# Performance work log

Measured on AMD Instinct MI355X. Metric: run time of the kernel, lower is better.

## Reference

```python
import jax, jax.numpy as jnp
import numpy as np

NUM_NETWORKS = 1024
IN_FEATURES = 32
OUT_FEATURES = 32
POINTS_PER_NET = 128
TOTAL_POINTS = NUM_NETWORKS * POINTS_PER_NET  # 131072


def setup_inputs() -> dict:
    key = jax.random.key(0)
    k1, k2, k3 = jax.random.split(key, 3)
    x = jax.random.normal(k1, (TOTAL_POINTS, IN_FEATURES), dtype=jnp.float32)
    # per-network weight matrices [N, in, out] and biases [N, out]
    weights = jax.random.normal(k2, (NUM_NETWORKS, IN_FEATURES, OUT_FEATURES), dtype=jnp.float32) * 0.1
    biases = jax.random.normal(k3, (NUM_NETWORKS, OUT_FEATURES), dtype=jnp.float32) * 0.1
    # contiguous point counts per network (static/uniform here, matching sum == TOTAL_POINTS)
    batch_size_per_network = jnp.full((NUM_NETWORKS,), POINTS_PER_NET, dtype=jnp.int32)
    return {"x": x, "weights": weights, "biases": biases,
            "batch_size_per_network": batch_size_per_network}


def reference(x, weights, biases, batch_size_per_network):
    # Grouped batched matmul: points are laid out contiguously per network.
    # seg[t] = network id owning point t.
    n = weights.shape[0]
    total = x.shape[0]
    seg = jnp.repeat(jnp.arange(n, dtype=jnp.int32), batch_size_per_network,
                     total_repeat_length=total)  # [total]
    # y_t = x_t @ W[seg_t] + b[seg_t]
    w_t = weights[seg]                     # [total, in, out] (gathered per point)
    y = jnp.einsum('ti,tio->to', x, w_t) + biases[seg]
    return y
```

## Files before the change

kernel.cpp:

```cpp
#include <hip/hip_runtime.h>


#define BLK 128

__global__ __launch_bounds__(BLK) void mnl_kernel(
    const float* __restrict__ x,
    const float* __restrict__ w,
    const float* __restrict__ bias,
    const int* __restrict__ cnt,
    float* __restrict__ y)
{
    __shared__ float xT[32][BLK];
    __shared__ float Wl[32][32];
    __shared__ float Bl[32];
    __shared__ int   red[BLK];

    const int n = blockIdx.x;
    const int t = threadIdx.x;

    int s = 0;
    for (int j = t; j < n; j += BLK) s += cnt[j];
    red[t] = s;
    __syncthreads();
    #pragma unroll
    for (int off = BLK / 2; off > 0; off >>= 1) {
        if (t < off) red[t] += red[t + off];
        __syncthreads();
    }
    const int base  = red[0];
    const int count = cnt[n];

    {
        const float4* wg  = reinterpret_cast<const float4*>(w + (size_t)n * 1024);
        float4*       wl4 = reinterpret_cast<float4*>(&Wl[0][0]);
        wl4[t]       = wg[t];
        wl4[t + BLK] = wg[t + BLK];
        if (t < 8) {
            reinterpret_cast<float4*>(Bl)[t] =
                reinterpret_cast<const float4*>(bias + (size_t)n * 32)[t];
        }
    }

    const int o0 = (t & 7) * 4;
    const int p0 = (t >> 3) * 8;

    for (int pc = 0; pc < count; pc += BLK) {
        const int p = pc + t;
        float4 rr[8];
        if (p < count) {
            const float4* xg = reinterpret_cast<const float4*>(x + (size_t)(base + p) * 32);
            #pragma unroll
            for (int k = 0; k < 8; ++k) rr[k] = xg[k];
        } else {
            #pragma unroll
            for (int k = 0; k < 8; ++k) rr[k] = make_float4(0.f, 0.f, 0.f, 0.f);
        }

        __syncthreads();

        #pragma unroll
        for (int k = 0; k < 8; ++k) {
            xT[4 * k + 0][t] = rr[k].x;
            xT[4 * k + 1][t] = rr[k].y;
            xT[4 * k + 2][t] = rr[k].z;
            xT[4 * k + 3][t] = rr[k].w;
        }

        __syncthreads();

        float acc[8][4] = {};
        #pragma unroll
        for (int i = 0; i < 32; ++i) {
            const float4 xa = *reinterpret_cast<const float4*>(&xT[i][p0]);
            const float4 xb = *reinterpret_cast<const float4*>(&xT[i][p0 + 4]);
            const float4 wv = *reinterpret_cast<const float4*>(&Wl[i][o0]);
            const float xs[8] = {xa.x, xa.y, xa.z, xa.w, xb.x, xb.y, xb.z, xb.w};
            const float ws[4] = {wv.x, wv.y, wv.z, wv.w};
            #pragma unroll
            for (int pp = 0; pp < 8; ++pp)
                #pragma unroll
                for (int oo = 0; oo < 4; ++oo)
                    acc[pp][oo] = fmaf(xs[pp], ws[oo], acc[pp][oo]);
        }

        const float4 b4 = *reinterpret_cast<const float4*>(&Bl[o0]);
        #pragma unroll
        for (int pp = 0; pp < 8; ++pp) {
            const int prow = pc + p0 + pp;
            if (prow < count) {
                float4 o;
                o.x = acc[pp][0] + b4.x;
                o.y = acc[pp][1] + b4.y;
                o.z = acc[pp][2] + b4.z;
                o.w = acc[pp][3] + b4.w;
                *reinterpret_cast<float4*>(&y[(size_t)(base + prow) * 32 + o0]) = o;
            }
        }
    }
}

extern "C" void kernel_launch(void* const* d_in, const int* in_sizes, int n_in,
                              void* d_out, int out_size, void* d_ws, size_t ws_size,
                              hipStream_t stream) {
    const float* x    = (const float*)d_in[0];
    const float* w    = (const float*)d_in[1];
    const float* bias = (const float*)d_in[2];
    const int*   cnt  = (const int*)d_in[3];
    float*       y    = (float*)d_out;
    const int n_nets = in_sizes[3];

    mnl_kernel<<<n_nets, BLK, 0, stream>>>(x, w, bias, cnt, y);
}
```

Before: 18.47 us.

## Compute one full output row per thread with weights read directly from global

Replaces the shared-memory transpose and tiled 8x4 micro-kernel with a per-thread row computation. Each thread loads its 32-float input row, reads the network's weights and bias straight from global (uniform across the block, so they are cached scalar/broadcast loads), and writes a full output row. The prefix-sum reduction now uses wavefront shuffles instead of a shared-memory tree, which drops most barriers. The tradeoff is per-thread strided row accesses to x and y, which coalesce poorly, and heavy register use (about 64 values live per thread).

```diff
diff --git a/kernel.cpp b/kernel.cpp
--- a/kernel.cpp
+++ b/kernel.cpp
@@ -10,92 +10,55 @@
     const int* __restrict__ cnt,
     float* __restrict__ y)
 {
-    __shared__ float xT[32][BLK];
-    __shared__ float Wl[32][32];
-    __shared__ float Bl[32];
-    __shared__ int   red[BLK];
-
     const int n = blockIdx.x;
     const int t = threadIdx.x;
 
     int s = 0;
     for (int j = t; j < n; j += BLK) s += cnt[j];
-    red[t] = s;
+    #pragma unroll
+    for (int off = 32; off > 0; off >>= 1) s += __shfl_xor(s, off, 64);
+    __shared__ int sb[BLK / 64];
+    if ((t & 63) == 0) sb[t >> 6] = s;
     __syncthreads();
+    int base = 0;
     #pragma unroll
-    for (int off = BLK / 2; off > 0; off >>= 1) {
-        if (t < off) red[t] += red[t + off];
-        __syncthreads();
-    }
-    const int base  = red[0];
+    for (int wv = 0; wv < BLK / 64; ++wv) base += sb[wv];
+
     const int count = cnt[n];
+    const float* __restrict__ wn = w + (size_t)n * (32 * 32);
+    const float* __restrict__ bn = bias + (size_t)n * 32;
 
-    {
-        const float4* wg  = reinterpret_cast<const float4*>(w + (size_t)n * 1024);
-        float4*       wl4 = reinterpret_cast<float4*>(&Wl[0][0]);
-        wl4[t]       = wg[t];
-        wl4[t + BLK] = wg[t + BLK];
-        if (t < 8) {
-            reinterpret_cast<float4*>(Bl)[t] =
-                reinterpret_cast<const float4*>(bias + (size_t)n * 32)[t];
-        }
-    }
-
-    const int o0 = (t & 7) * 4;
-    const int p0 = (t >> 3) * 8;
-
-    for (int pc = 0; pc < count; pc += BLK) {
-        const int p = pc + t;
-        float4 rr[8];
-        if (p < count) {
-            const float4* xg = reinterpret_cast<const float4*>(x + (size_t)(base + p) * 32);
-            #pragma unroll
-            for (int k = 0; k < 8; ++k) rr[k] = xg[k];
-        } else {
-            #pragma unroll
-            for (int k = 0; k < 8; ++k) rr[k] = make_float4(0.f, 0.f, 0.f, 0.f);
+    for (int p = t; p < count; p += BLK) {
+        const float4* __restrict__ xr =
+            reinterpret_cast<const float4*>(x + (size_t)(base + p) * 32);
+        float xv[32];
+        #pragma unroll
+        for (int k = 0; k < 8; ++k) {
+            const float4 v = xr[k];
+            xv[4 * k + 0] = v.x;
+            xv[4 * k + 1] = v.y;
+            xv[4 * k + 2] = v.z;
+            xv[4 * k + 3] = v.w;
         }
 
-        __syncthreads();
+        float acc[32];
+        #pragma unroll
+        for (int o = 0; o < 32; ++o) acc[o] = bn[o];
 
         #pragma unroll
-        for (int k = 0; k < 8; ++k) {
-            xT[4 * k + 0][t] = rr[k].x;
-            xT[4 * k + 1][t] = rr[k].y;
-            xT[4 * k + 2][t] = rr[k].z;
-            xT[4 * k + 3][t] = rr[k].w;
+        for (int i = 0; i < 32; ++i) {
+            const float xi = xv[i];
+            #pragma unroll
+            for (int o = 0; o < 32; ++o)
+                acc[o] = fmaf(xi, wn[i * 32 + o], acc[o]);
         }
 
-        __syncthreads();
-
-        float acc[8][4] = {};
+        float4* __restrict__ yr =
+            reinterpret_cast<float4*>(y + (size_t)(base + p) * 32);
         #pragma unroll
-        for (int i = 0; i < 32; ++i) {
-            const float4 xa = *reinterpret_cast<const float4*>(&xT[i][p0]);
-            const float4 xb = *reinterpret_cast<const float4*>(&xT[i][p0 + 4]);
-            const float4 wv = *reinterpret_cast<const float4*>(&Wl[i][o0]);
-            const float xs[8] = {xa.x, xa.y, xa.z, xa.w, xb.x, xb.y, xb.z, xb.w};
-            const float ws[4] = {wv.x, wv.y, wv.z, wv.w};
-            #pragma unroll
-            for (int pp = 0; pp < 8; ++pp)
-                #pragma unroll
-                for (int oo = 0; oo < 4; ++oo)
-                    acc[pp][oo] = fmaf(xs[pp], ws[oo], acc[pp][oo]);
-        }
-
-        const float4 b4 = *reinterpret_cast<const float4*>(&Bl[o0]);
-        #pragma unroll
-        for (int pp = 0; pp < 8; ++pp) {
-            const int prow = pc + p0 + pp;
-            if (prow < count) {
-                float4 o;
-                o.x = acc[pp][0] + b4.x;
-                o.y = acc[pp][1] + b4.y;
-                o.z = acc[pp][2] + b4.z;
-                o.w = acc[pp][3] + b4.w;
-                *reinterpret_cast<float4*>(&y[(size_t)(base + prow) * 32 + o0]) = o;
-            }
-        }
+        for (int k = 0; k < 8; ++k)
+            yr[k] = make_float4(acc[4 * k + 0], acc[4 * k + 1],
+                                acc[4 * k + 2], acc[4 * k + 3]);
     }
 }
 
@@ -107,7 +70,7 @@
     const float* bias = (const float*)d_in[2];
     const int*   cnt  = (const int*)d_in[3];
     float*       y    = (float*)d_out;
-    const int n_nets = in_sizes[3];
+    const int n_nets  = in_sizes[3];
 
     mnl_kernel<<<n_nets, BLK, 0, stream>>>(x, w, bias, cnt, y);
 }
```

Measured after the change: 34.76 us. +88.2%, slower.

## Split each network across two 64-thread blocks and use wavefront shuffle reduction

Applied to the files above, without the earlier changes.

Launches two single-wavefront blocks per network, each handling alternating 64-point chunks. The shared-memory tree reduction for the prefix offset becomes a wavefront xor-shuffle reduction, which removes several barriers. Weight and bias loads are issued into registers before the prefix-sum loop so their latency overlaps it, and the bias is read straight from global memory. In exchange, each network's weights and the prefix scan over counts are fetched twice, once per block.

```diff
diff --git a/kernel.cpp b/kernel.cpp
--- a/kernel.cpp
+++ b/kernel.cpp
@@ -1,54 +1,55 @@
 #include <hip/hip_runtime.h>
 
 
-#define BLK 128
+#define NT 64
 
-__global__ __launch_bounds__(BLK) void mnl_kernel(
+__global__ __launch_bounds__(NT) void mnl_kernel(
     const float* __restrict__ x,
     const float* __restrict__ w,
     const float* __restrict__ bias,
     const int* __restrict__ cnt,
     float* __restrict__ y)
 {
-    __shared__ float xT[32][BLK];
+    __shared__ float xT[32][NT];
     __shared__ float Wl[32][32];
-    __shared__ float Bl[32];
-    __shared__ int   red[BLK];
 
-    const int n = blockIdx.x;
+    const int b = blockIdx.x;
+    const int n = b >> 1;
+    const int h = b & 1;
     const int t = threadIdx.x;
 
-    int s = 0;
-    for (int j = t; j < n; j += BLK) s += cnt[j];
-    red[t] = s;
-    __syncthreads();
-    #pragma unroll
-    for (int off = BLK / 2; off > 0; off >>= 1) {
-        if (t < off) red[t] += red[t + off];
-        __syncthreads();
-    }
-    const int base  = red[0];
-    const int count = cnt[n];
-
-    {
-        const float4* wg  = reinterpret_cast<const float4*>(w + (size_t)n * 1024);
-        float4*       wl4 = reinterpret_cast<float4*>(&Wl[0][0]);
-        wl4[t]       = wg[t];
-        wl4[t + BLK] = wg[t + BLK];
-        if (t < 8) {
-            reinterpret_cast<float4*>(Bl)[t] =
-                reinterpret_cast<const float4*>(bias + (size_t)n * 32)[t];
-        }
-    }
+    const float4* __restrict__ wg = reinterpret_cast<const float4*>(w + (size_t)n * 1024);
+    const float4 wr0 = wg[t];
+    const float4 wr1 = wg[t + 64];
+    const float4 wr2 = wg[t + 128];
+    const float4 wr3 = wg[t + 192];
 
     const int o0 = (t & 7) * 4;
     const int p0 = (t >> 3) * 8;
 
-    for (int pc = 0; pc < count; pc += BLK) {
+    const float4 b4 = *reinterpret_cast<const float4*>(bias + (size_t)n * 32 + o0);
+
+    int s = 0;
+    for (int j = t; j < n; j += NT) s += cnt[j];
+    #pragma unroll
+    for (int off = 32; off > 0; off >>= 1) s += __shfl_xor(s, off, 64);
+    const int base  = s;
+    const int count = cnt[n];
+
+    {
+        float4* wl4 = reinterpret_cast<float4*>(&Wl[0][0]);
+        wl4[t]       = wr0;
+        wl4[t + 64]  = wr1;
+        wl4[t + 128] = wr2;
+        wl4[t + 192] = wr3;
+    }
+
+    for (int pc = h * NT; pc < count; pc += 2 * NT) {
         const int p = pc + t;
         float4 rr[8];
         if (p < count) {
-            const float4* xg = reinterpret_cast<const float4*>(x + (size_t)(base + p) * 32);
+            const float4* __restrict__ xg =
+                reinterpret_cast<const float4*>(x + (size_t)(base + p) * 32);
             #pragma unroll
             for (int k = 0; k < 8; ++k) rr[k] = xg[k];
         } else {
@@ -83,7 +84,6 @@
                     acc[pp][oo] = fmaf(xs[pp], ws[oo], acc[pp][oo]);
         }
 
-        const float4 b4 = *reinterpret_cast<const float4*>(&Bl[o0]);
         #pragma unroll
         for (int pp = 0; pp < 8; ++pp) {
             const int prow = pc + p0 + pp;
@@ -107,7 +107,7 @@
     const float* bias = (const float*)d_in[2];
     const int*   cnt  = (const int*)d_in[3];
     float*       y    = (float*)d_out;
-    const int n_nets = in_sizes[3];
+    const int n_nets  = in_sizes[3];
 
-    mnl_kernel<<<n_nets, BLK, 0, stream>>>(x, w, bias, cnt, y);
+    mnl_kernel<<<2 * n_nets, NT, 0, stream>>>(x, w, bias, cnt, y);
 }
```

Measured after the change: 19.05 us. 3.1% more time.
